# Kernel optimization log

Hardware: AMD Instinct MI355X
Metric: run time of the kernel (lower is better)

## Reference

```python
import jax, jax.numpy as jnp
import numpy as np

T = 37          # bio_type_num
LP = T + 2      # padded label size (start, end)
START, END = T, T + 1


def crf_loglik(logits, labels, lens, trans):
    # logits: [B,S,LP] padded scores; labels: [B,S] ints; lens: [B]; trans[to, from]: [LP,LP]
    B, S, Lp = logits.shape
    dt = logits.dtype
    tpos = jnp.arange(S)
    mask = (tpos[None, :] < lens[:, None]).astype(dt)  # [B,S]
    # unary gold score
    unary = jnp.take_along_axis(logits, labels[..., None], axis=2)[..., 0] * mask
    # binary (transition) gold score with start/end extension
    labels_ext = jnp.concatenate([
        jnp.full((B, 1), START, labels.dtype), labels, jnp.full((B, 1), END, labels.dtype)], axis=1)  # [B,S+2]
    pos = jnp.arange(S + 2)
    labels_ext = jnp.where(pos[None, :] < (lens + 1)[:, None], labels_ext, END)
    frm, to = labels_ext[:, :-1], labels_ext[:, 1:]          # [B,S+1]
    trn_scr = trans[to, frm]                                  # [B,S+1]
    m2 = (jnp.arange(S + 1)[None, :] < (lens + 1)[:, None]).astype(dt)
    gold = unary.sum(1) + (trn_scr * m2).sum(1)               # [B]
    # partition function: forward algorithm (sequential scan over time)
    alpha0 = jnp.full((B, Lp), -100.0, dt).at[:, START].set(0.0)
    def step(alpha, xt):
        logit_t, m_t = xt                                     # [B,Lp], [B] bool
        mat = logit_t[:, :, None] + alpha[:, None, :] + trans[None, :, :]  # [B,to,from]
        alpha_nxt = jax.nn.logsumexp(mat, axis=2)
        alpha = jnp.where(m_t[:, None], alpha_nxt, alpha)
        return alpha, None
    xs = (jnp.swapaxes(logits, 0, 1), (tpos[None, :] < lens[:, None]).T)
    alpha, _ = jax.lax.scan(step, alpha0, xs)
    alpha = alpha + trans[END][None, :]
    norm = jax.nn.logsumexp(alpha, axis=1)                    # [B]
    return gold - norm


def ner_forward(h, bio_embed, W_cat, b_cat, W_crf, b_crf, transition, token_nums, entity_seq_labels):
    B, S, H = h.shape
    scale = 1.0 / jnp.sqrt(jnp.asarray(H, h.dtype))
    # one-head attention: query=token states, key=value=bio type embeddings (mask all ones -> no-op)
    scores = jnp.einsum('bsh,th->bst', h, bio_embed) * scale  # [B,S,T]
    attn = jax.nn.softmax(scores, axis=-1)
    aware = jnp.einsum('bst,th->bsh', attn, bio_embed)        # [B,S,H]
    x = jnp.concatenate([h, aware, h * aware], axis=-1)       # [B,S,3H]
    x = jax.nn.gelu(x @ W_cat + b_cat, approximate=False)     # [B,S,H]
    logits = x @ W_crf + b_crf                                # [B,S,T]
    pads = jnp.full((B, S, 2), -10000.0, logits.dtype)
    ner_scores = jnp.concatenate([logits, pads], axis=-1)     # [B,S,LP]
    ner_loss = crf_loglik(ner_scores, entity_seq_labels, token_nums, transition)
    return ner_scores, ner_loss


def setup_inputs() -> dict:
    key = jax.random.key(0)
    ks = jax.random.split(key, 8)
    B, S, H = 32, 512, 1024
    token_hidden_states = jax.random.normal(ks[0], (B, S, H), jnp.float32)
    token_masks = jnp.ones((B, S), jnp.bool_)
    token_nums = jax.random.randint(ks[1], (B,), 256, S + 1).at[0].set(S)
    entity_seq_labels = jax.random.randint(ks[2], (B, S), 0, T)
    bio_embed = jax.random.normal(ks[3], (T, H), jnp.float32) * 0.02
    W_cat = jax.random.normal(ks[4], (3 * H, H), jnp.float32) * (3.0 * H) ** -0.5
    b_cat = jnp.zeros((H,), jnp.float32)
    W_crf = jax.random.normal(ks[5], (H, T), jnp.float32) * H ** -0.5
    b_crf = jnp.zeros((T,), jnp.float32)
    transition = jax.random.normal(ks[6], (LP, LP), jnp.float32)
    return {
        'token_hidden_states': token_hidden_states, 'token_masks': token_masks,
        'token_nums': token_nums, 'entity_seq_labels': entity_seq_labels,
        'bio_embed': bio_embed, 'W_cat': W_cat, 'b_cat': b_cat,
        'W_crf': W_crf, 'b_crf': b_crf, 'transition': transition,
    }


def reference(token_hidden_states, token_masks, token_nums, entity_seq_labels,
              bio_embed, W_cat, b_cat, W_crf, b_crf, transition):
    # token_masks only generates an all-ones bio mask in the original (no-op); dropout in eval mode.
    return ner_forward(token_hidden_states, bio_embed, W_cat, b_cat, W_crf, b_crf,
                       transition, token_nums, entity_seq_labels)
```

## Files before the change

kernel.cpp:

```cpp
#include <hip/hip_runtime.h>
#include <hip/hip_bf16.h>
#include <math.h>

#define NB 32
#define NS 512
#define NH 1024
#define NT 37
#define NLP 39
#define NM (NB*NS)

typedef __attribute__((ext_vector_type(8))) short bf16x8;
typedef __attribute__((ext_vector_type(4))) float f32x4;

__device__ __forceinline__ float bf2f(unsigned int u) {
    unsigned int x = u << 16;
    float f;
    __builtin_memcpy(&f, &x, 4);
    return f;
}
__device__ __forceinline__ unsigned short f2bf(float f) {
    __hip_bfloat16 hb = __float2bfloat16(f);
    unsigned short u;
    __builtin_memcpy(&u, &hb, 2);
    return u;
}
__device__ __forceinline__ unsigned int pk2(float lo, float hi) {
    return ((unsigned int)f2bf(hi) << 16) | (unsigned int)f2bf(lo);
}
__device__ __forceinline__ int SW64(int b)  { return b ^ ((b >> 2) & 0x70); }
__device__ __forceinline__ int TSW(int row, int kcolByte) {
    return (row * 128 + kcolByte) ^ ((row & 7) << 4);
}
__device__ __forceinline__ float rl(float x, int l) {
    return __int_as_float(__builtin_amdgcn_readlane(__float_as_int(x), l));
}
__device__ __forceinline__ void gld16(const void* g, void* l) {
    __builtin_amdgcn_global_load_lds((const __attribute__((address_space(1))) void*)g,
                                     (__attribute__((address_space(3))) void*)l, 16, 0, 0);
}
#define VMW(N) asm volatile("s_waitcnt vmcnt(" #N ")" ::: "memory")
#define BARR() do { __builtin_amdgcn_s_barrier(); __builtin_amdgcn_sched_barrier(0); } while (0)

__global__ __launch_bounds__(256) void kPre(const float* __restrict__ h,
                                            const float* __restrict__ bio,
                                            const float* __restrict__ Wcat,
                                            const float* __restrict__ Wcrf,
                                            unsigned short* __restrict__ attn,
                                            char* __restrict__ Asw,
                                            char* __restrict__ Wsw,
                                            unsigned short* __restrict__ WT) {
    __shared__ __align__(16) char shmem[48 * 2048];
    const int bid = blockIdx.x;
    const int tid = threadIdx.x;

    if (bid < 256) {
        char* Bl = shmem;
        const int lane = tid & 63;
        const int wid  = tid >> 6;
        const int lr   = lane & 15;
        const int lk   = lane >> 4;
        const int m0   = bid * 64;
        const int tm   = bid >> 1;
        const int rbase = (bid & 1) * 64 + wid * 16 + lr;

        for (int idx = tid; idx < 37 * 256; idx += 256) {
            int t = idx >> 8, k4 = idx & 255;
            float4 v = *(const float4*)&bio[(size_t)t * NH + k4 * 4];
            int byte = (t * 2048 + k4 * 8) ^ ((t & 7) << 4);
            *(uint2*)(Bl + byte) = make_uint2(pk2(v.x, v.y), pk2(v.z, v.w));
        }
        for (int idx = tid; idx < 11 * 256; idx += 256) {
            int t = 37 + (idx >> 8), k4 = idx & 255;
            int byte = (t * 2048 + k4 * 8) ^ ((t & 7) << 4);
            *(uint2*)(Bl + byte) = make_uint2(0, 0);
        }
        __syncthreads();

        const int arow = m0 + wid * 16 + lr;
        const float* hp = h + (size_t)arow * NH + lk * 8;

        f32x4 sacc[3];
#pragma unroll
        for (int j = 0; j < 3; ++j) sacc[j] = (f32x4){0.f, 0.f, 0.f, 0.f};

        float4 p0 = *(const float4*)(hp);
        float4 p1 = *(const float4*)(hp + 4);
        for (int kt = 0; kt < NH; kt += 32) {
            float4 c0 = p0, c1 = p1;
            if (kt + 32 < NH) {
                p0 = *(const float4*)(hp + kt + 32);
                p1 = *(const float4*)(hp + kt + 36);
            }
            union { unsigned int u[4]; bf16x8 v; uint4 q; } af;
            af.u[0] = pk2(c0.x, c0.y); af.u[1] = pk2(c0.z, c0.w);
            af.u[2] = pk2(c1.x, c1.y); af.u[3] = pk2(c1.z, c1.w);
            {
                int kg = kt + lk * 8;
                size_t tb = ((size_t)tm * 48 + (kg >> 6)) * 16384;
                *(uint4*)(Asw + tb + TSW(rbase, (kg & 63) * 2)) = af.q;
            }
#pragma unroll
            for (int nf = 0; nf < 3; ++nf) {
                int t = nf * 16 + lr;
                int byte = (t * 2048 + (kt + lk * 8) * 2) ^ ((t & 7) << 4);
                bf16x8 bf = *(const bf16x8*)(Bl + byte);
                sacc[nf] = __builtin_amdgcn_mfma_f32_16x16x32_bf16(af.v, bf, sacc[nf], 0, 0, 0);
            }
        }

#pragma unroll
        for (int r = 0; r < 4; ++r) {
            const int orow = wid * 16 + lk * 4 + r;
            float s0 = sacc[0][r] * 0.03125f;
            float s1 = sacc[1][r] * 0.03125f;
            float s2 = sacc[2][r] * 0.03125f;
            const bool v2 = (lr < 5);
            float mx = fmaxf(fmaxf(s0, s1), v2 ? s2 : -1e30f);
#pragma unroll
            for (int d = 1; d < 16; d <<= 1) mx = fmaxf(mx, __shfl_xor(mx, d, 64));
            float e0 = __expf(s0 - mx), e1 = __expf(s1 - mx);
            float e2 = v2 ? __expf(s2 - mx) : 0.f;
            float sm = e0 + e1 + e2;
#pragma unroll
            for (int d = 1; d < 16; d <<= 1) sm += __shfl_xor(sm, d, 64);
            float inv = 1.f / sm;
            size_t g = (size_t)(m0 + orow) * 64;
            attn[g + lr]      = f2bf(e0 * inv);
            attn[g + 16 + lr] = f2bf(e1 * inv);
            attn[g + 32 + lr] = f2bf(e2 * inv);
            attn[g + 48 + lr] = 0;
        }
    } else if (bid < 640) {
        unsigned short* wt = (unsigned short*)shmem;
        const int tile = bid - 256;
        const int tn   = tile / 48;
        const int tk   = tile - tn * 48;
        const int n00  = tn * 128;
        const int k0   = tk * 64;

        for (int lin = tid; lin < 2048; lin += 256) {
            int kk = lin >> 5, ng = lin & 31;
            float4 v = *(const float4*)&Wcat[(size_t)(k0 + kk) * NH + n00 + ng * 4];
            *(uint2*)&wt[kk * 128 + ng * 4] = make_uint2(pk2(v.x, v.y), pk2(v.z, v.w));
        }
        __syncthreads();
        for (int lin = tid; lin < 1024; lin += 256) {
            int rn = lin >> 3, kg = lin & 7;
            unsigned short t8[8];
#pragma unroll
            for (int j = 0; j < 8; ++j) t8[j] = wt[(kg * 8 + j) * 128 + rn];
            uint4 v;
            __builtin_memcpy(&v, t8, 16);
            *(uint4*)(Wsw + (size_t)tile * 16384 + TSW(rn, kg * 16)) = v;
        }
    } else {
        const int idx = (bid - 640) * 256 + tid;
        if (idx < 48 * 384) {
            const int t = idx / 384, kg = idx - t * 384;
            unsigned short v[8];
#pragma unroll
            for (int e = 0; e < 8; ++e) {
                int k = kg * 8 + e;
                v[e] = (t < NT) ? f2bf(Wcrf[(size_t)k * NT + t]) : (unsigned short)0;
            }
            uint4 w;
            __builtin_memcpy(&w, v, 16);
            *(uint4*)(WT + (size_t)t * 3072 + kg * 8) = w;
        }
    }
}

__global__ __launch_bounds__(512) void kA1(const float* __restrict__ h,
                                           const float* __restrict__ bio,
                                           unsigned short* __restrict__ attn) {
    __shared__ __align__(16) char Bl[48 * 2048];

    const int tid  = threadIdx.x;
    const int lane = tid & 63;
    const int wid  = tid >> 6;
    const int lr   = lane & 15;
    const int lk   = lane >> 4;
    const int m0   = blockIdx.x * 128;

    for (int idx = tid; idx < 37 * 256; idx += 512) {
        int t = idx >> 8, k4 = idx & 255;
        float4 v = *(const float4*)&bio[(size_t)t * NH + k4 * 4];
        int byte = (t * 2048 + k4 * 8) ^ ((t & 7) << 4);
        *(uint2*)(Bl + byte) = make_uint2(pk2(v.x, v.y), pk2(v.z, v.w));
    }
    for (int idx = tid; idx < 11 * 256; idx += 512) {
        int t = 37 + (idx >> 8), k4 = idx & 255;
        int byte = (t * 2048 + k4 * 8) ^ ((t & 7) << 4);
        *(uint2*)(Bl + byte) = make_uint2(0, 0);
    }
    __syncthreads();

    const int arow = m0 + wid * 16 + lr;
    const float* hp = h + (size_t)arow * NH + lk * 8;

    f32x4 sacc[3];
#pragma unroll
    for (int j = 0; j < 3; ++j) sacc[j] = (f32x4){0.f, 0.f, 0.f, 0.f};

    float4 p0 = *(const float4*)(hp);
    float4 p1 = *(const float4*)(hp + 4);
    for (int kt = 0; kt < NH; kt += 32) {
        float4 c0 = p0, c1 = p1;
        if (kt + 32 < NH) {
            p0 = *(const float4*)(hp + kt + 32);
            p1 = *(const float4*)(hp + kt + 36);
        }
        union { unsigned int u[4]; bf16x8 v; } af;
        af.u[0] = pk2(c0.x, c0.y); af.u[1] = pk2(c0.z, c0.w);
        af.u[2] = pk2(c1.x, c1.y); af.u[3] = pk2(c1.z, c1.w);
#pragma unroll
        for (int nf = 0; nf < 3; ++nf) {
            int t = nf * 16 + lr;
            int byte = (t * 2048 + (kt + lk * 8) * 2) ^ ((t & 7) << 4);
            bf16x8 bf = *(const bf16x8*)(Bl + byte);
            sacc[nf] = __builtin_amdgcn_mfma_f32_16x16x32_bf16(af.v, bf, sacc[nf], 0, 0, 0);
        }
    }

#pragma unroll
    for (int r = 0; r < 4; ++r) {
        const int orow = wid * 16 + lk * 4 + r;
        float s0 = sacc[0][r] * 0.03125f;
        float s1 = sacc[1][r] * 0.03125f;
        float s2 = sacc[2][r] * 0.03125f;
        const bool v2 = (lr < 5);
        float mx = fmaxf(fmaxf(s0, s1), v2 ? s2 : -1e30f);
#pragma unroll
        for (int d = 1; d < 16; d <<= 1) mx = fmaxf(mx, __shfl_xor(mx, d, 64));
        float e0 = __expf(s0 - mx), e1 = __expf(s1 - mx);
        float e2 = v2 ? __expf(s2 - mx) : 0.f;
        float sm = e0 + e1 + e2;
#pragma unroll
        for (int d = 1; d < 16; d <<= 1) sm += __shfl_xor(sm, d, 64);
        float inv = 1.f / sm;
        size_t g = (size_t)(m0 + orow) * 64;
        attn[g + lr]      = f2bf(e0 * inv);
        attn[g + 16 + lr] = f2bf(e1 * inv);
        attn[g + 32 + lr] = f2bf(e2 * inv);
        attn[g + 48 + lr] = 0;
    }
}

__global__ __launch_bounds__(256) void kA2(const unsigned short* __restrict__ attn,
                                           const float* __restrict__ bio,
                                           unsigned short* __restrict__ aware) {
    __shared__ __align__(16) char Bsl[128 * 64];

    const int tid  = threadIdx.x;
    const int lane = tid & 63;
    const int wid  = tid >> 6;
    const int wm   = (wid >> 1) * 64;
    const int wn   = (wid & 1) * 64;
    const int lr   = lane & 15;
    const int lk   = lane >> 4;
    const int n0   = blockIdx.x * 128;
    const int m0   = blockIdx.y * 128;

    const int bn = tid & 127;
    const int bq = (tid >> 7) * 16;

    f32x4 acc[4][4];
#pragma unroll
    for (int i = 0; i < 4; ++i)
#pragma unroll
        for (int j = 0; j < 4; ++j) acc[i][j] = (f32x4){0.f, 0.f, 0.f, 0.f};

#pragma unroll
    for (int ks = 0; ks < 2; ++ks) {
        unsigned int p[8];
#pragma unroll
        for (int i = 0; i < 8; ++i) {
            int t0 = ks*32 + bq + 2*i;
            float lo = (t0     < NT) ? bio[(size_t)t0 * NH + n0 + bn]       : 0.f;
            float hi = (t0 + 1 < NT) ? bio[(size_t)(t0+1) * NH + n0 + bn]   : 0.f;
            p[i] = pk2(lo, hi);
        }
        __syncthreads();
        *(int4*)(Bsl + SW64(bn*64 + bq*2))      = make_int4(p[0], p[1], p[2], p[3]);
        *(int4*)(Bsl + SW64(bn*64 + bq*2 + 16)) = make_int4(p[4], p[5], p[6], p[7]);
        __syncthreads();

        bf16x8 af[4];
#pragma unroll
        for (int mf = 0; mf < 4; ++mf)
            af[mf] = *(const bf16x8*)(attn + (size_t)(m0 + wm + mf*16 + lr) * 64 + ks*32 + lk*8);
#pragma unroll
        for (int nf = 0; nf < 4; ++nf) {
            bf16x8 bb = *(const bf16x8*)(Bsl + SW64((wn + nf*16 + lr)*64 + lk*16));
#pragma unroll
            for (int mf = 0; mf < 4; ++mf)
                acc[mf][nf] = __builtin_amdgcn_mfma_f32_16x16x32_bf16(af[mf], bb, acc[mf][nf], 0, 0, 0);
        }
    }

#pragma unroll
    for (int mf = 0; mf < 4; ++mf)
#pragma unroll
        for (int nf = 0; nf < 4; ++nf)
#pragma unroll
            for (int r = 0; r < 4; ++r) {
                size_t row = (size_t)(m0 + wm + mf*16 + lk*4 + r);
                aware[row * NH + n0 + wn + nf*16 + lr] = f2bf(acc[mf][nf][r]);
            }
}

__global__ __launch_bounds__(256) void kA2f(const unsigned short* __restrict__ attn,
                                            const float* __restrict__ bio,
                                            char* __restrict__ Asw) {
    __shared__ __align__(16) char Bsl[128 * 64];
    __shared__ __align__(16) unsigned short awL[128 * 128];

    const int tid  = threadIdx.x;
    const int lane = tid & 63;
    const int wid  = tid >> 6;
    const int wm   = (wid >> 1) * 64;
    const int wn   = (wid & 1) * 64;
    const int lr   = lane & 15;
    const int lk   = lane >> 4;
    const int n0   = blockIdx.x * 128;
    const int m0   = blockIdx.y * 128;
    const int tm   = blockIdx.y;

    const int bn = tid & 127;
    const int bq = (tid >> 7) * 16;

    f32x4 acc[4][4];
#pragma unroll
    for (int i = 0; i < 4; ++i)
#pragma unroll
        for (int j = 0; j < 4; ++j) acc[i][j] = (f32x4){0.f, 0.f, 0.f, 0.f};

#pragma unroll
    for (int ks = 0; ks < 2; ++ks) {
        unsigned int p[8];
#pragma unroll
        for (int i = 0; i < 8; ++i) {
            int t0 = ks*32 + bq + 2*i;
            float lo = (t0     < NT) ? bio[(size_t)t0 * NH + n0 + bn]       : 0.f;
            float hi = (t0 + 1 < NT) ? bio[(size_t)(t0+1) * NH + n0 + bn]   : 0.f;
            p[i] = pk2(lo, hi);
        }
        __syncthreads();
        *(int4*)(Bsl + SW64(bn*64 + bq*2))      = make_int4(p[0], p[1], p[2], p[3]);
        *(int4*)(Bsl + SW64(bn*64 + bq*2 + 16)) = make_int4(p[4], p[5], p[6], p[7]);
        __syncthreads();

        bf16x8 af[4];
#pragma unroll
        for (int mf = 0; mf < 4; ++mf)
            af[mf] = *(const bf16x8*)(attn + (size_t)(m0 + wm + mf*16 + lr) * 64 + ks*32 + lk*8);
#pragma unroll
        for (int nf = 0; nf < 4; ++nf) {
            bf16x8 bb = *(const bf16x8*)(Bsl + SW64((wn + nf*16 + lr)*64 + lk*16));
#pragma unroll
            for (int mf = 0; mf < 4; ++mf)
                acc[mf][nf] = __builtin_amdgcn_mfma_f32_16x16x32_bf16(af[mf], bb, acc[mf][nf], 0, 0, 0);
        }
    }

#pragma unroll
    for (int mf = 0; mf < 4; ++mf)
#pragma unroll
        for (int nf = 0; nf < 4; ++nf)
#pragma unroll
            for (int r = 0; r < 4; ++r)
                awL[(wm + mf*16 + lk*4 + r) * 128 + wn + nf*16 + lr] = f2bf(acc[mf][nf][r]);
    __syncthreads();

#pragma unroll
    for (int i = 0; i < 8; ++i) {
        int lin = tid + i * 256;
        int row = lin >> 4, kg = lin & 15;
        uint4 v = *(const uint4*)&awL[row * 128 + kg * 8];
        int kglob = 1024 + n0 + kg * 8;
        size_t tbase = ((size_t)tm * 48 + (kglob >> 6)) * 16384;
        *(uint4*)(Asw + tbase + TSW(row, (kglob & 63) * 2)) = v;
    }
#pragma unroll
    for (int i = 0; i < 8; ++i) {
        int lin = tid + i * 256;
        int row = lin >> 4, kg = lin & 15;
        int k0g = n0 + kg * 8;
        size_t tb0 = ((size_t)tm * 48 + (k0g >> 6)) * 16384;
        uint4 hv4 = *(const uint4*)(Asw + tb0 + TSW(row, (k0g & 63) * 2));
        unsigned int hu[4] = {hv4.x, hv4.y, hv4.z, hv4.w};
        uint4 awv = *(const uint4*)&awL[row * 128 + kg * 8];
        unsigned int awu[4] = {awv.x, awv.y, awv.z, awv.w};
        unsigned int p2[4];
#pragma unroll
        for (int j = 0; j < 4; ++j) {
            float lo = bf2f(hu[j] & 0xffffu) * bf2f(awu[j] & 0xffffu);
            float hi = bf2f(hu[j] >> 16)     * bf2f(awu[j] >> 16);
            p2[j] = pk2(lo, hi);
        }
        int k2g = 2048 + n0 + kg * 8;
        size_t tb2 = ((size_t)tm * 48 + (k2g >> 6)) * 16384;
        *(uint4*)(Asw + tb2 + TSW(row, (k2g & 63) * 2)) = make_uint4(p2[0], p2[1], p2[2], p2[3]);
    }
}

__global__ __launch_bounds__(512, 2) void kBf(const char* __restrict__ Asw,
                                              const char* __restrict__ Wsw,
                                              const float* __restrict__ bcat,
                                              const unsigned short* __restrict__ WT,
                                              float* __restrict__ P) {
    __shared__ __align__(16) char lds[131072];

    const int tid  = threadIdx.x;
    const int lane = tid & 63;
    const int wid  = tid >> 6;
    const int widm = wid >> 2;
    const int widn = wid & 3;
    const int lr   = lane & 15;
    const int lk   = lane >> 4;

    const int id   = blockIdx.x;
    const int xcd  = id & 7;
    const int slot = id >> 3;
    const int Mt   = xcd * 8 + (slot >> 2);
    const int Nt   = slot & 3;
    const int m0   = Mt * 256, n0 = Nt * 256;
    const int soff = tid * 16;

    f32x4 acc00[4][2], acc01[4][2], acc10[4][2], acc11[4][2];
#pragma unroll
    for (int i = 0; i < 4; ++i)
#pragma unroll
        for (int j = 0; j < 2; ++j) {
            acc00[i][j] = (f32x4){0.f,0.f,0.f,0.f};
            acc01[i][j] = (f32x4){0.f,0.f,0.f,0.f};
            acc10[i][j] = (f32x4){0.f,0.f,0.f,0.f};
            acc11[i][j] = (f32x4){0.f,0.f,0.f,0.f};
        }

    auto stageHalf = [&](int T, int ph) {
        const bool isA = (ph == 0) || (ph == 3);
        const int  h   = isA ? (ph == 3 ? 1 : 0) : (ph - 1);
        const char* src = isA
            ? Asw + ((size_t)((2*Mt + h) * 48 + T)) * 16384
            : Wsw + ((size_t)((2*Nt + h) * 48 + T)) * 16384;
        char* dst = lds + (isA ? 0 : 65536) + (T & 1) * 32768 + h * 16384;
        gld16(src + soff,        dst + soff);
        gld16(src + soff + 8192, dst + soff + 8192);
    };
    auto loadA = [&](bf16x8 (&af)[4][2], int q, int half) {
        const char* base = lds + q * 32768 + half * 16384;
#pragma unroll
        for (int i = 0; i < 4; ++i) {
            int row = widm * 64 + i * 16 + lr;
#pragma unroll
            for (int kk = 0; kk < 2; ++kk)
                af[i][kk] = *(const bf16x8*)(base + TSW(row, kk * 64 + lk * 16));
        }
    };
    auto loadB = [&](bf16x8 (&bfr)[2][2], int q, int half) {
        const char* base = lds + 65536 + q * 32768 + half * 16384;
#pragma unroll
        for (int j = 0; j < 2; ++j) {
            int col = widn * 32 + j * 16 + lr;
#pragma unroll
            for (int kk = 0; kk < 2; ++kk)
                bfr[j][kk] = *(const bf16x8*)(base + TSW(col, kk * 64 + lk * 16));
        }
    };
    auto mma = [&](f32x4 (&ac)[4][2], bf16x8 (&af)[4][2], bf16x8 (&bfr)[2][2]) {
        __builtin_amdgcn_s_setprio(1);
#pragma unroll
        for (int kk = 0; kk < 2; ++kk)
#pragma unroll
            for (int i = 0; i < 4; ++i)
#pragma unroll
                for (int j = 0; j < 2; ++j)
                    ac[i][j] = __builtin_amdgcn_mfma_f32_16x16x32_bf16(
                        af[i][kk], bfr[j][kk], ac[i][j], 0, 0, 0);
        __builtin_amdgcn_s_setprio(0);
    };

    stageHalf(0, 0); stageHalf(0, 1); stageHalf(0, 2); stageHalf(0, 3);
    VMW(0);
    BARR();

    for (int T = 0; T < 47; ++T) {
        const int q = T & 1;
        bf16x8 af0[4][2], af1[4][2], bf0[2][2], bf1[2][2];
        stageHalf(T + 1, 0);
        VMW(6);
        BARR();
        loadA(af0, q, 0); loadB(bf0, q, 0);
        mma(acc00, af0, bf0);
        stageHalf(T + 1, 1);
        VMW(6);
        BARR();
        loadB(bf1, q, 1);
        mma(acc01, af0, bf1);
        stageHalf(T + 1, 2);
        VMW(6);
        BARR();
        loadA(af1, q, 1);
        mma(acc10, af1, bf0);
        stageHalf(T + 1, 3);
        BARR();
        mma(acc11, af1, bf1);
    }
    {
        const int q = 1;
        bf16x8 af0[4][2], af1[4][2], bf0[2][2], bf1[2][2];
        VMW(4);
        BARR();
        loadA(af0, q, 0); loadB(bf0, q, 0);
        mma(acc00, af0, bf0);
        VMW(2);
        BARR();
        loadB(bf1, q, 1);
        mma(acc01, af0, bf1);
        VMW(0);
        BARR();
        loadA(af1, q, 1);
        mma(acc10, af1, bf0);
        BARR();
        mma(acc11, af1, bf1);
    }

    __syncthreads();
    auto stashQ = [&](f32x4 (&ac)[4][2], int a, int b) {
#pragma unroll
        for (int j = 0; j < 2; ++j) {
            const int lcol = b * 128 + widn * 32 + j * 16 + lr;
            const int kc = lcol >> 6, kk = lcol & 63;
            const float bc = bcat[n0 + lcol];
#pragma unroll
            for (int i = 0; i < 4; ++i)
#pragma unroll
                for (int r = 0; r < 4; ++r) {
                    int lrow = a * 128 + widm * 64 + i * 16 + lk * 4 + r;
                    float x = ac[i][j][r] + bc;
                    float g = 0.5f * x * (1.0f + erff(x * 0.70710678118654752f));
                    *(unsigned short*)(lds + kc * 32768 + TSW(lrow, kk * 2)) = f2bf(g);
                }
        }
    };
    stashQ(acc00, 0, 0); stashQ(acc01, 0, 1); stashQ(acc10, 1, 0); stashQ(acc11, 1, 1);
    __syncthreads();

    bf16x8 wfrag[3][8];
#pragma unroll
    for (int tt = 0; tt < 3; ++tt) {
        const int t = tt * 16 + lr;
#pragma unroll
        for (int ks = 0; ks < 8; ++ks)
            wfrag[tt][ks] = *(const bf16x8*)(WT + (size_t)t * 3072 + n0 + ks * 32 + lk * 8);
    }

    f32x4 pacc[2][3];
#pragma unroll
    for (int i = 0; i < 2; ++i)
#pragma unroll
        for (int j = 0; j < 3; ++j) pacc[i][j] = (f32x4){0.f, 0.f, 0.f, 0.f};
#pragma unroll
    for (int rt2 = 0; rt2 < 2; ++rt2) {
        const int lrow = wid * 32 + rt2 * 16 + lr;
#pragma unroll
        for (int ks = 0; ks < 8; ++ks) {
            const int kc = ks >> 1, kh = ks & 1;
            bf16x8 af = *(const bf16x8*)(lds + kc * 32768 + TSW(lrow, kh * 64 + lk * 16));
#pragma unroll
            for (int tt = 0; tt < 3; ++tt)
                pacc[rt2][tt] = __builtin_amdgcn_mfma_f32_16x16x32_bf16(
                    af, wfrag[tt][ks], pacc[rt2][tt], 0, 0, 0);
        }
    }

    float* Pb = P + (size_t)Nt * NM * 48;
#pragma unroll
    for (int rt2 = 0; rt2 < 2; ++rt2)
#pragma unroll
        for (int tt = 0; tt < 3; ++tt)
#pragma unroll
            for (int r = 0; r < 4; ++r) {
                int row = Mt * 256 + wid * 32 + rt2 * 16 + lk * 4 + r;
                Pb[(size_t)row * 48 + tt * 16 + lr] = pacc[rt2][tt][r];
            }
}

__global__ __launch_bounds__(256) void kDmCr(const float* __restrict__ P,
                                             const float* __restrict__ bcrf,
                                             const int* __restrict__ lens,
                                             const float* __restrict__ trans,
                                             float* __restrict__ out,
                                             float* __restrict__ Pm,
                                             float* __restrict__ Pc) {
    __shared__ float el_all[64 * 64];
    __shared__ __align__(16) char Mb[2 * 6144];

    const int tid = threadIdx.x;
    const int b   = blockIdx.x >> 3;
    const int s   = blockIdx.x & 7;
    const int t0  = s * 64;
    const size_t STRIDE = (size_t)NM * 48;

    {
        const int i  = tid >> 2;
        const int tg = (tid & 3) * 12;
        const int gr = b * NS + t0 + i;
#pragma unroll
        for (int j = 0; j < 12; ++j) {
            int t = tg + j;
            size_t flat = (size_t)gr * 48 + t;
            float v = P[flat] + P[STRIDE + flat] + P[2*STRIDE + flat] + P[3*STRIDE + flat];
            float o, el;
            if (t < NT) { o = v + bcrf[t]; el = __expf(o); }
            else        { o = -10000.0f;   el = 0.f; }
            if (t < NLP) out[(size_t)gr * NLP + t] = o;
            el_all[i * 64 + t] = el;
        }
    }
    for (int z = tid; z < 64 * 16; z += 256)
        el_all[(z >> 4) * 64 + 48 + (z & 15)] = 0.f;
    __syncthreads();

    if (tid >= 64) return;

    const int lane = tid;
    const int lr   = lane & 15;
    const int lk   = lane >> 4;
    const int len  = lens[b];
    const int nsteps = (len > t0) ? ((len - t0 < 64) ? (len - t0) : 64) : 0;
    float* Pg = Pm + (size_t)(b * 8 + s) * 2304;

    if (nsteps == 0) {
        for (int j = 0; j < 36; ++j) Pg[j * 64 + lane] = 0.f;
        if (lane < 48) Pg[lane * 48 + lane] = 1.f;
        if (lane == 0) Pc[b * 8 + s] = 0.f;
        return;
    }

    bf16x8 Tf[3][2];
#pragma unroll
    for (int tt = 0; tt < 3; ++tt)
#pragma unroll
        for (int ks = 0; ks < 2; ++ks) {
            const int row = tt * 16 + lr;
            unsigned int u[4];
#pragma unroll
            for (int e2 = 0; e2 < 4; ++e2) {
                int f0 = ks * 32 + lk * 8 + 2 * e2;
                float lo = (row < NLP && f0     < NLP) ? __expf(trans[row * NLP + f0])     : 0.f;
                float hi = (row < NLP && f0 + 1 < NLP) ? __expf(trans[row * NLP + f0 + 1]) : 0.f;
                u[e2] = pk2(lo, hi);
            }
            union { unsigned int uu[4]; bf16x8 v; } cv;
            cv.uu[0]=u[0]; cv.uu[1]=u[1]; cv.uu[2]=u[2]; cv.uu[3]=u[3];
            Tf[tt][ks] = cv.v;
        }

    for (int j = 0; j < 48; ++j)
        *(unsigned int*)(Mb + j * 256 + lane * 4) = 0;
    if (lane < 48) {
        int byte = (lane * 128 + lane * 2) ^ ((lane & 7) << 4);
        *(unsigned short*)(Mb + byte) = f2bf(1.0f);
    }

    float Cacc = 0.f;

    for (int i = 0; i < nsteps; ++i) {
        const int q = i & 1;
        const char* Mr = Mb + q * 6144;

        bf16x8 Bf[3][2];
#pragma unroll
        for (int ct = 0; ct < 3; ++ct) {
#pragma unroll
            for (int ks = 0; ks < 2; ++ks) {
                int col = ct * 16 + lr;
                int byte = (col * 128 + (ks * 32 + lk * 8) * 2) ^ ((col & 7) << 4);
                Bf[ct][ks] = *(const bf16x8*)(Mr + byte);
            }
        }
        f32x4 el4[3];
#pragma unroll
        for (int tt = 0; tt < 3; ++tt)
            el4[tt] = *(const f32x4*)&el_all[i * 64 + tt * 16 + lk * 4];

        f32x4 c[3][3];
#pragma unroll
        for (int tt = 0; tt < 3; ++tt)
#pragma unroll
            for (int ct = 0; ct < 3; ++ct) {
                c[tt][ct] = __builtin_amdgcn_mfma_f32_16x16x32_bf16(
                    Tf[tt][0], Bf[ct][0], (f32x4){0.f,0.f,0.f,0.f}, 0, 0, 0);
                c[tt][ct] = __builtin_amdgcn_mfma_f32_16x16x32_bf16(
                    Tf[tt][1], Bf[ct][1], c[tt][ct], 0, 0, 0);
            }
#pragma unroll
        for (int tt = 0; tt < 3; ++tt)
#pragma unroll
            for (int ct = 0; ct < 3; ++ct)
#pragma unroll
                for (int r = 0; r < 4; ++r)
                    c[tt][ct][r] *= el4[tt][r];

        if ((i & 3) == 3) {
            float sv = rl(c[0][0][0], 0);
            float rr = __builtin_amdgcn_rcpf(sv);
#pragma unroll
            for (int tt = 0; tt < 3; ++tt)
#pragma unroll
                for (int ct = 0; ct < 3; ++ct)
#pragma unroll
                    for (int r = 0; r < 4; ++r) c[tt][ct][r] *= rr;
            Cacc -= __logf(rr);
        }

        if (i == nsteps - 1) {
#pragma unroll
            for (int tt = 0; tt < 3; ++tt)
#pragma unroll
                for (int ct = 0; ct < 3; ++ct)
#pragma unroll
                    for (int r = 0; r < 4; ++r) {
                        int row = tt * 16 + lk * 4 + r;
                        int col = ct * 16 + lr;
                        Pg[row * 48 + col] = c[tt][ct][r];
                    }
        } else {
            char* Mw = Mb + (q ^ 1) * 6144;
#pragma unroll
            for (int tt = 0; tt < 3; ++tt)
#pragma unroll
                for (int ct = 0; ct < 3; ++ct) {
                    int col = ct * 16 + lr;
                    int k   = tt * 16 + lk * 4;
                    int byte = (col * 128 + k * 2) ^ ((col & 7) << 4);
                    *(uint2*)(Mw + byte) = make_uint2(pk2(c[tt][ct][0], c[tt][ct][1]),
                                                      pk2(c[tt][ct][2], c[tt][ct][3]));
                }
        }
    }

    if (lane == 0) Pc[b * 8 + s] = Cacc;
}

__global__ __launch_bounds__(256) void kDc(const float* __restrict__ scores,
                                           const int* __restrict__ labels,
                                           const int* __restrict__ lens,
                                           const float* __restrict__ trans,
                                           const float* __restrict__ Pm,
                                           const float* __restrict__ Pc,
                                           float* __restrict__ loss) {
    __shared__ float trL[39 * 41];
    __shared__ float gred[4];

    const int b    = blockIdx.x;
    const int tid  = threadIdx.x;
    const int lane = tid & 63;
    const int wid  = tid >> 6;
    const int len  = lens[b];
    const float* sb = scores + (size_t)b * NS * NLP;

    for (int idx = tid; idx < 39 * 39; idx += 256) {
        int to = idx / 39, f = idx - to * 39;
        trL[to * 41 + f] = trans[idx];
    }
    __syncthreads();

    float g = 0.0f;
    for (int t = tid; t < len; t += 256) g += sb[(size_t)t * NLP + labels[b * NS + t]];
    for (int i = tid; i <= len; i += 256) {
        int frm = (i == 0) ? 37 : labels[b * NS + i - 1];
        int to  = (i == len) ? 38 : labels[b * NS + i];
        g += trL[to * 41 + frm];
    }
#pragma unroll
    for (int off = 32; off > 0; off >>= 1) g += __shfl_xor(g, off, 64);
    if (lane == 0) gred[wid] = g;
    __syncthreads();

    if (wid != 0) return;

    const float gold = (gred[0] + gred[1]) + (gred[2] + gred[3]);
    const bool act48 = (lane < 48);

    const float* P0 = Pm + (size_t)b * 8 * 2304;
    float v = act48 ? P0[lane * 48 + 37] : 0.f;
    float C = Pc[b * 8];

    for (int s = 1; s < 8; ++s) {
        float as_[40];
#pragma unroll
        for (int f = 0; f < 40; ++f) as_[f] = rl(v, f);
        __builtin_amdgcn_sched_barrier(0);
        const float* Ps = Pm + (size_t)(b * 8 + s) * 2304;
        float c = 0.f;
        if (act48) {
            const float4* rowp = (const float4*)(Ps + lane * 48);
#pragma unroll
            for (int q = 0; q < 10; ++q) {
                float4 rv = rowp[q];
                c = fmaf(rv.x, as_[q*4+0], c);
                c = fmaf(rv.y, as_[q*4+1], c);
                c = fmaf(rv.z, as_[q*4+2], c);
                c = fmaf(rv.w, as_[q*4+3], c);
            }
        }
        float sv = rl(c, 0);
        float rr = __builtin_amdgcn_rcpf(sv);
        v = c * rr;
        C -= __logf(rr);
        C += Pc[b * 8 + s];
    }

    const float trEnd = (lane < NLP) ? trL[38 * 41 + lane] : 0.f;
    float aend = (lane < NLP && v > 0.f) ? C + __logf(v) + trEnd : -1e30f;
    float mx = aend;
#pragma unroll
    for (int off = 32; off > 0; off >>= 1) mx = fmaxf(mx, __shfl_xor(mx, off, 64));
    float es = (lane < NLP) ? __expf(aend - mx) : 0.f;
#pragma unroll
    for (int off = 32; off > 0; off >>= 1) es += __shfl_xor(es, off, 64);
    float norm = mx + __logf(es);

    if (lane == 0) loss[b] = gold - norm;
}

__global__ __launch_bounds__(256) void kB(const float* __restrict__ h,
                                          const unsigned short* __restrict__ aware,
                                          const float* __restrict__ Wcat,
                                          const float* __restrict__ bcat,
                                          unsigned short* __restrict__ x2) {
    __shared__ __align__(16) char lds[16384];
    char* Asl = lds;
    char* Bsl = lds + 8192;

    const int tid  = threadIdx.x;
    const int lane = tid & 63;
    const int wid  = tid >> 6;
    const int wm   = (wid >> 1) * 64;
    const int wn   = (wid & 1) * 64;
    const int lr   = lane & 15;
    const int lk   = lane >> 4;

    const int id   = blockIdx.x;
    const int xcd  = id & 7;
    const int slot = id >> 3;
    const int m0   = (xcd * 16 + (slot >> 3)) * 128;
    const int n0   = (slot & 7) * 128;

    const int am = tid >> 1;
    const int ak = (tid & 1) * 16;
    const int bn = tid & 127;
    const int bk = (tid >> 7) * 16;

    f32x4 acc[4][4];
#pragma unroll
    for (int i = 0; i < 4; ++i)
#pragma unroll
        for (int j = 0; j < 4; ++j) acc[i][j] = (f32x4){0.f, 0.f, 0.f, 0.f};

    const float*          hrow = h     + (size_t)(m0 + am) * NH + ak;
    const unsigned short* arow = aware + (size_t)(m0 + am) * NH + ak;
    const float*          wcol = Wcat  + (size_t)bk * NH + n0 + bn;

    float hv[16];
    unsigned int aw[8];
    float wv[16];

    auto stage = [&](int kt) {
        const int region = kt >> 10;
        const int kb = kt & 1023;
        if (region != 1) {
            const float4* hp = (const float4*)(hrow + kb);
            float4 a = hp[0], b = hp[1], c = hp[2], d = hp[3];
            hv[0]=a.x; hv[1]=a.y; hv[2]=a.z; hv[3]=a.w;
            hv[4]=b.x; hv[5]=b.y; hv[6]=b.z; hv[7]=b.w;
            hv[8]=c.x; hv[9]=c.y; hv[10]=c.z; hv[11]=c.w;
            hv[12]=d.x; hv[13]=d.y; hv[14]=d.z; hv[15]=d.w;
        }
        if (region >= 1) {
            const uint4* ap = (const uint4*)(arow + kb);
            uint4 a0 = ap[0], a1 = ap[1];
            aw[0]=a0.x; aw[1]=a0.y; aw[2]=a0.z; aw[3]=a0.w;
            aw[4]=a1.x; aw[5]=a1.y; aw[6]=a1.z; aw[7]=a1.w;
        }
        {
            const float* wp = wcol + (size_t)kt * NH;
#pragma unroll
            for (int j = 0; j < 16; ++j) wv[j] = wp[(size_t)j * NH];
        }
    };

    auto writeStage = [&](int kt) {
        const int region = kt >> 10;
        unsigned int p[8];
        if (region == 0) {
#pragma unroll
            for (int i = 0; i < 8; ++i) p[i] = pk2(hv[2*i], hv[2*i+1]);
        } else if (region == 1) {
#pragma unroll
            for (int i = 0; i < 8; ++i) p[i] = aw[i];
        } else {
#pragma unroll
            for (int i = 0; i < 8; ++i) {
                float lo = hv[2*i]   * bf2f(aw[i] & 0xffffu);
                float hi = hv[2*i+1] * bf2f(aw[i] >> 16);
                p[i] = pk2(lo, hi);
            }
        }
        *(int4*)(Asl + SW64(am*64 + ak*2))      = make_int4(p[0], p[1], p[2], p[3]);
        *(int4*)(Asl + SW64(am*64 + ak*2 + 16)) = make_int4(p[4], p[5], p[6], p[7]);
        unsigned int q[8];
#pragma unroll
        for (int i = 0; i < 8; ++i) q[i] = pk2(wv[2*i], wv[2*i+1]);
        *(int4*)(Bsl + SW64(bn*64 + bk*2))      = make_int4(q[0], q[1], q[2], q[3]);
        *(int4*)(Bsl + SW64(bn*64 + bk*2 + 16)) = make_int4(q[4], q[5], q[6], q[7]);
    };

    stage(0);
    for (int kt = 0; kt < 3072; kt += 32) {
        __syncthreads();
        writeStage(kt);
        __syncthreads();
        if (kt + 32 < 3072) stage(kt + 32);

        bf16x8 af[4], bfr[4];
#pragma unroll
        for (int mf = 0; mf < 4; ++mf)
            af[mf] = *(const bf16x8*)(Asl + SW64((wm + mf*16 + lr)*64 + lk*16));
#pragma unroll
        for (int nf = 0; nf < 4; ++nf)
            bfr[nf] = *(const bf16x8*)(Bsl + SW64((wn + nf*16 + lr)*64 + lk*16));
#pragma unroll
        for (int mf = 0; mf < 4; ++mf)
#pragma unroll
            for (int nf = 0; nf < 4; ++nf)
                acc[mf][nf] = __builtin_amdgcn_mfma_f32_16x16x32_bf16(af[mf], bfr[nf], acc[mf][nf], 0, 0, 0);
    }

#pragma unroll
    for (int nf = 0; nf < 4; ++nf) {
        const int col = n0 + wn + nf*16 + lr;
        const float bc = bcat[col];
#pragma unroll
        for (int mf = 0; mf < 4; ++mf)
#pragma unroll
            for (int r = 0; r < 4; ++r) {
                size_t row = (size_t)(m0 + wm + mf*16 + lk*4 + r);
                float x = acc[mf][nf][r] + bc;
                float g = 0.5f * x * (1.0f + erff(x * 0.70710678118654752f));
                x2[row * NH + col] = f2bf(g);
            }
    }
}

__global__ __launch_bounds__(256) void kC(const unsigned short* __restrict__ x2,
                                          const float* __restrict__ Wcrf,
                                          const float* __restrict__ bcrf,
                                          float* __restrict__ out) {
    __shared__ __align__(16) char Asl[8192];
    __shared__ __align__(16) char Bsl[3072];

    const int tid  = threadIdx.x;
    const int lane = tid & 63;
    const int wid  = tid >> 6;
    const int lr   = lane & 15;
    const int lk   = lane >> 4;
    const int m0   = blockIdx.x * 128;
    const int am   = tid >> 1;
    const int ak   = (tid & 1) * 16;

    for (int i = tid; i < 192; i += 256) *(int4*)(Bsl + i*16) = make_int4(0, 0, 0, 0);

    f32x4 acc[2][3];
#pragma unroll
    for (int i = 0; i < 2; ++i)
#pragma unroll
        for (int j = 0; j < 3; ++j) acc[i][j] = (f32x4){0.f, 0.f, 0.f, 0.f};

    const unsigned short* xrow = x2 + (size_t)(m0 + am) * NH + ak;

    for (int kt = 0; kt < NH; kt += 32) {
        const uint4* xp = (const uint4*)(xrow + kt);
        uint4 x0 = xp[0], x1 = xp[1];
        float wv[5];
#pragma unroll
        for (int p = 0; p < 5; ++p) {
            int i = tid + p * 256;
            wv[p] = (i < 32*NT) ? Wcrf[(size_t)kt * NT + i] : 0.f;
        }
        __syncthreads();
        *(uint4*)(Asl + SW64(am*64 + ak*2))      = x0;
        *(uint4*)(Asl + SW64(am*64 + ak*2 + 16)) = x1;
#pragma unroll
        for (int p = 0; p < 5; ++p) {
            int i = tid + p * 256;
            if (i < 32*NT) {
                int kk = i / NT;
                int t  = i - kk * NT;
                *(unsigned short*)(Bsl + SW64(t*64 + kk*2)) = f2bf(wv[p]);
            }
        }
        __syncthreads();
        bf16x8 af[2], bfr[3];
#pragma unroll
        for (int mf = 0; mf < 2; ++mf)
            af[mf] = *(const bf16x8*)(Asl + SW64((wid*32 + mf*16 + lr)*64 + lk*16));
#pragma unroll
        for (int nf = 0; nf < 3; ++nf)
            bfr[nf] = *(const bf16x8*)(Bsl + SW64((nf*16 + lr)*64 + lk*16));
#pragma unroll
        for (int mf = 0; mf < 2; ++mf)
#pragma unroll
            for (int nf = 0; nf < 3; ++nf)
                acc[mf][nf] = __builtin_amdgcn_mfma_f32_16x16x32_bf16(af[mf], bfr[nf], acc[mf][nf], 0, 0, 0);
    }

#pragma unroll
    for (int nf = 0; nf < 3; ++nf) {
        const int t = nf*16 + lr;
        const float bc = (t < NT) ? bcrf[t] : 0.f;
#pragma unroll
        for (int mf = 0; mf < 2; ++mf)
#pragma unroll
            for (int r = 0; r < 4; ++r) {
                size_t row = (size_t)(m0 + wid*32 + mf*16 + lk*4 + r);
                if (t < NT)       out[row * NLP + t] = acc[mf][nf][r] + bc;
                else if (t < NLP) out[row * NLP + t] = -10000.0f;
            }
    }
}

#define CRFSTEP(EL) do {                                   \
    float as_[37];                                         \
    _Pragma("unroll")                                      \
    for (int f_ = 0; f_ < 37; ++f_) as_[f_] = rl(a, f_);   \
    __builtin_amdgcn_sched_barrier(0);                     \
    float c0 = 0.f, c1 = 0.f, c2 = 0.f, c3 = 0.f;          \
    _Pragma("unroll")                                      \
    for (int f_ = 0; f_ < 36; f_ += 4) {                   \
        c0 = fmaf(as_[f_    ], trow[f_    ], c0);          \
        c1 = fmaf(as_[f_ + 1], trow[f_ + 1], c1);          \
        c2 = fmaf(as_[f_ + 2], trow[f_ + 2], c2);          \
        c3 = fmaf(as_[f_ + 3], trow[f_ + 3], c3);          \
    }                                                      \
    c0 = fmaf(as_[36], trow[36], c0);                      \
    a = (EL) * ((c0 + c1) + (c2 + c3));                    \
} while (0)

__global__ __launch_bounds__(256) void kDold(const float* __restrict__ scores,
                                             const int* __restrict__ labels,
                                             const int* __restrict__ lens,
                                             const float* __restrict__ trans,
                                             float* __restrict__ loss) {
    __shared__ float S[NS * NLP];
    __shared__ float trL[39 * 41];
    __shared__ int   labL[NS];
    __shared__ float gred[4];

    const int b    = blockIdx.x;
    const int tid  = threadIdx.x;
    const int lane = tid & 63;
    const int wid  = tid >> 6;
    const int len  = lens[b];
    const float* sb = scores + (size_t)b * NS * NLP;

    {
        const int n4 = (len * NLP + 3) >> 2;
        const float4* src = (const float4*)sb;
        float4* dst = (float4*)S;
        for (int i = tid; i < n4; i += 256) dst[i] = src[i];
    }
    for (int i = tid; i < NS; i += 256) labL[i] = labels[b * NS + i];
    for (int idx = tid; idx < 39 * 39; idx += 256) {
        int to = idx / 39, f = idx - to * 39;
        trL[to * 41 + f] = trans[idx];
    }
    __syncthreads();

    float g = 0.0f;
    for (int t = tid; t < len; t += 256) g += S[t * NLP + labL[t]];
    for (int i = tid; i <= len; i += 256) {
        int frm = (i == 0) ? 37 : labL[i - 1];
        int to  = (i == len) ? 38 : labL[i];
        g += trL[to * 41 + frm];
    }
#pragma unroll
    for (int off = 32; off > 0; off >>= 1) g += __shfl_xor(g, off, 64);
    if (lane == 0) gred[wid] = g;
    __syncthreads();

    if (wid != 0) return;

    const float gold = (gred[0] + gred[1]) + (gred[2] + gred[3]);

    const int myrow = (lane < 39) ? lane : 0;
    float trow[39];
#pragma unroll
    for (int f = 0; f < 39; ++f) trow[f] = __expf(trL[myrow * 41 + f]);
    const float trEnd = (lane < 39) ? trL[38 * 41 + lane] : 0.f;
    const bool act = (lane < 39);

    float l0 = act ? S[lane] : -10000.f;
    float a = act ? __expf(l0) * trow[37] : 0.f;
    float C = 0.0f;

    auto ldrow = [&](int r) {
        r = (r < len) ? r : (len - 1);
        return S[act ? (r * NLP + lane) : 0];
    };
    float lg0 = ldrow(1), lg1 = ldrow(2), lg2 = ldrow(3), lg3 = ldrow(4);

    int t = 1;
    for (; t + 3 < len; t += 4) {
        float e0 = __expf(lg0), e1 = __expf(lg1), e2 = __expf(lg2), e3 = __expf(lg3);
        lg0 = ldrow(t + 4); lg1 = ldrow(t + 5); lg2 = ldrow(t + 6); lg3 = ldrow(t + 7);
        CRFSTEP(e0); CRFSTEP(e1); CRFSTEP(e2); CRFSTEP(e3);
        float s = rl(a, 0);
        float rr = __builtin_amdgcn_rcpf(s);
        a *= rr; C -= __logf(rr);
    }
    for (; t < len; ++t) {
        float el = __expf(ldrow(t));
        CRFSTEP(el);
    }

    float aend = (act && a > 0.f) ? C + __logf(a) + trEnd : -1e30f;
    float mx = aend;
#pragma unroll
    for (int off = 32; off > 0; off >>= 1) mx = fmaxf(mx, __shfl_xor(mx, off, 64));
    float es = act ? __expf(aend - mx) : 0.0f;
#pragma unroll
    for (int off = 32; off > 0; off >>= 1) es += __shfl_xor(es, off, 64);
    float norm = mx + __logf(es);

    if (lane == 0) loss[b] = gold - norm;
}

extern "C" void kernel_launch(void* const* d_in, const int* in_sizes, int n_in,
                              void* d_out, int out_size, void* d_ws, size_t ws_size,
                              hipStream_t stream) {
    const float* h        = (const float*)d_in[0];
    const int* token_nums = (const int*)d_in[2];
    const int* labels     = (const int*)d_in[3];
    const float* bio      = (const float*)d_in[4];
    const float* Wcat     = (const float*)d_in[5];
    const float* bcat     = (const float*)d_in[6];
    const float* Wcrf     = (const float*)d_in[7];
    const float* bcrf     = (const float*)d_in[8];
    const float* trans    = (const float*)d_in[9];

    float* out = (float*)d_out;
    unsigned short* attn  = (unsigned short*)d_out;

    const size_t ASW_BYTES = (size_t)128 * 48 * 16384;
    const size_t P_BYTES   = (size_t)4 * NM * 48 * 4;
    const size_t WSW_BYTES = (size_t)8 * 48 * 16384;
    const size_t WT_BYTES  = (size_t)48 * 3072 * 2;
    const size_t PM_BYTES  = (size_t)NB * 8 * 2304 * 4;
    const size_t PC_BYTES  = (size_t)NB * 8 * 4;
    const bool fast = ws_size >= ASW_BYTES + P_BYTES + WSW_BYTES + WT_BYTES + PM_BYTES + PC_BYTES;

    if (fast) {
        char*  Asw = (char*)d_ws;
        float* P   = (float*)((char*)d_ws + ASW_BYTES);
        char*  Wsw = (char*)d_ws + ASW_BYTES + P_BYTES;
        unsigned short* WT = (unsigned short*)((char*)d_ws + ASW_BYTES + P_BYTES + WSW_BYTES);
        float* Pm  = (float*)((char*)d_ws + ASW_BYTES + P_BYTES + WSW_BYTES + WT_BYTES);
        float* Pc  = Pm + (size_t)NB * 8 * 2304;

        hipLaunchKernelGGL(kPre, dim3(712), dim3(256), 0, stream,
                           h, bio, Wcat, Wcrf, attn, Asw, Wsw, WT);
        hipLaunchKernelGGL(kA2f, dim3(NH / 128, NM / 128), dim3(256), 0, stream,
                           attn, bio, Asw);
        hipLaunchKernelGGL(kBf, dim3(256), dim3(512), 0, stream, Asw, Wsw, bcat, WT, P);
        hipLaunchKernelGGL(kDmCr, dim3(NB * 8), dim3(256), 0, stream,
                           P, bcrf, token_nums, trans, out, Pm, Pc);
        hipLaunchKernelGGL(kDc, dim3(NB), dim3(256), 0, stream, out, labels, token_nums,
                           trans, Pm, Pc, out + (size_t)NM * NLP);
    } else {
        unsigned short* aware = (unsigned short*)d_ws;
        unsigned short* x2    = aware + (size_t)NM * NH;

        hipLaunchKernelGGL(kA1, dim3(NM / 128), dim3(512), 0, stream, h, bio, attn);
        hipLaunchKernelGGL(kA2, dim3(NH / 128, NM / 128), dim3(256), 0, stream, attn, bio, aware);
        hipLaunchKernelGGL(kB, dim3((NH / 128) * (NM / 128)), dim3(256), 0, stream,
                           h, aware, Wcat, bcat, x2);
        hipLaunchKernelGGL(kC, dim3(NM / 128), dim3(256), 0, stream, x2, Wcrf, bcrf, out);
        hipLaunchKernelGGL(kDold, dim3(NB), dim3(256), 0, stream, out, labels, token_nums,
                           trans, out + (size_t)NM * NLP);
    }
}
```

Measured before the change: 213.9 us.

## Restructure GEMM main loop to one wait per iteration and fold epilogue

Reworks the double-buffered GEMM K-loop so that only one vmcnt wait and barrier pair guards each iteration's data. Fragment LDS reads are issued before the next global stage and barrier instead of after them. The separate tail iteration is folded into the loop using a prefetch predicate. This is meant to cut the per-quarter vmcnt stalls and let global loads overlap the MFMA work. The risk is that the buffer reuse ordering is now more subtle, and the added branching may change scheduling.

After: 212.6 us. Within noise of the previous version (-0.6%).

```diff
diff --git a/kernel.cpp b/kernel.cpp
--- a/kernel.cpp
+++ b/kernel.cpp
@@ -485,43 +485,34 @@
     VMW(0);
     BARR();
 
-    for (int T = 0; T < 47; ++T) {
+    for (int T = 0; T < 48; ++T) {
         const int q = T & 1;
+        const bool pf = (T + 1 < 48);
         bf16x8 af0[4][2], af1[4][2], bf0[2][2], bf1[2][2];
-        stageHalf(T + 1, 0);
-        VMW(6);
+
+        if (T > 0) {
+            if (pf) { stageHalf(T + 1, 0); VMW(2); }
+            else    { VMW(0); }
+            BARR();
+        } else if (pf) {
+            stageHalf(T + 1, 0);
+        }
+
+        loadA(af0, q, 0); loadB(bf0, q, 0);
+        if (pf) stageHalf(T + 1, 1);
         BARR();
-        loadA(af0, q, 0); loadB(bf0, q, 0);
         mma(acc00, af0, bf0);
-        stageHalf(T + 1, 1);
-        VMW(6);
+
+        loadB(bf1, q, 1);
+        if (pf) stageHalf(T + 1, 2);
         BARR();
-        loadB(bf1, q, 1);
         mma(acc01, af0, bf1);
-        stageHalf(T + 1, 2);
-        VMW(6);
+
+        loadA(af1, q, 1);
+        if (pf) stageHalf(T + 1, 3);
         BARR();
-        loadA(af1, q, 1);
         mma(acc10, af1, bf0);
-        stageHalf(T + 1, 3);
-        BARR();
-        mma(acc11, af1, bf1);
-    }
-    {
-        const int q = 1;
-        bf16x8 af0[4][2], af1[4][2], bf0[2][2], bf1[2][2];
-        VMW(4);
-        BARR();
-        loadA(af0, q, 0); loadB(bf0, q, 0);
-        mma(acc00, af0, bf0);
-        VMW(2);
-        BARR();
-        loadB(bf1, q, 1);
-        mma(acc01, af0, bf1);
-        VMW(0);
-        BARR();
-        loadA(af1, q, 1);
-        mma(acc10, af1, bf0);
+
         BARR();
         mma(acc11, af1, bf1);
     }
```
